# Optimization experiments

Hardware: AMD Instinct MI355X
Metric: run time of the kernel (lower is better)

Reference implementation:

```python
import jax, jax.numpy as jnp
import numpy as np

H, DK = 8, 32
D_MODEL = H * DK  # 256
Q_DIM = K_DIM = V_DIM = 256
B, T, S = 4, 4, 1024
NEG = -1e10


def setup_inputs() -> dict:
    rng = jax.random.key(0)
    ks = jax.random.split(rng, 12)
    w = lambda k, shp: (jax.random.normal(k, shp, jnp.float32) * 0.02)
    return {
        "query": jax.random.normal(ks[0], (B, T, S, Q_DIM), jnp.float32),
        "key": jax.random.normal(ks[1], (B, T, S, K_DIM), jnp.float32),
        "value": jax.random.normal(ks[2], (B, T, S, V_DIM), jnp.float32),
        "mask": jax.random.randint(ks[3], (B, T), 1, S + 1),  # valid lengths in [1, S]
        "Wq": w(ks[4], (D_MODEL, Q_DIM)), "bq": jnp.zeros((D_MODEL,), jnp.float32),
        "Wk": w(ks[5], (D_MODEL, K_DIM)), "bk": jnp.zeros((D_MODEL,), jnp.float32),
        "Wv": w(ks[6], (D_MODEL, V_DIM)), "bv": jnp.zeros((D_MODEL,), jnp.float32),
        "Wo": w(ks[7], (Q_DIM, D_MODEL)), "bo": jnp.zeros((Q_DIM,), jnp.float32),
    }


def reference(query, key, value, mask, Wq, bq, Wk, bk, Wv, bv, Wo, bo):
    b, t, s, _ = query.shape
    # projections -> [B,T,h,S,d_k]
    def proj(x, W, bias):
        y = jnp.einsum('btsf,df->btsd', x, W) + bias
        return y.reshape(b, t, s, H, DK).transpose(0, 1, 3, 2, 4)
    q = proj(query, Wq, bq)
    k = proj(key, Wk, bk)
    v = proj(value, Wv, bv)
    # scores [B,T,h,S,S]
    scores = jnp.einsum('bthqd,bthkd->bthqk', q, k) / jnp.sqrt(jnp.float32(DK))
    # vectorized length mask: positions < len on both axes (replaces torch python loop)
    valid = jnp.arange(s)[None, None, :] < mask[:, :, None]        # [B,T,S]
    m = valid[:, :, None, :, None] & valid[:, :, None, None, :]    # [B,T,1,S,S]
    scores = jnp.where(m, scores, NEG)
    p = jax.nn.softmax(scores, axis=-1)
    x = jnp.einsum('bthqk,bthkd->bthqd', p, v)                     # [B,T,h,S,d_k]
    x = x.transpose(0, 1, 3, 2, 4).reshape(b, t, s, H * DK)
    return jnp.einsum('btsd,qd->btsq', x, Wo) + bo
```

## Files before the change

### kernel.cpp

```cpp
#include <hip/hip_runtime.h>

#define EXPC 0.25505654442163f

typedef __attribute__((ext_vector_type(8))) short bfrag;
typedef __attribute__((ext_vector_type(4))) float ffrag;
typedef __attribute__((ext_vector_type(8))) unsigned int u8v;
typedef __attribute__((ext_vector_type(4))) unsigned int u4v;
typedef __attribute__((ext_vector_type(2))) unsigned int u2v;

__device__ __forceinline__ short f2bf(float x) {
  union { float f; unsigned u; } v; v.f = x;
  return (short)((v.u + 0x8000u) >> 16);
}

__device__ __forceinline__ unsigned int packbf(float a, float b) {
  return __builtin_amdgcn_perm(__float_as_uint(b) + 0x8000u,
                               __float_as_uint(a) + 0x8000u, 0x07060302u);
}

__device__ __forceinline__ bfrag cvtp(u8v x) {
  u4v r;
#pragma unroll
  for (int i = 0; i < 4; ++i)
    r[i] = __builtin_amdgcn_perm(x[2 * i + 1] + 0x8000u, x[2 * i] + 0x8000u, 0x07060302u);
  union { u4v u; bfrag b; } c; c.u = r; return c.b;
}
__device__ __forceinline__ bfrag cvt8(const float* __restrict__ p) {
  return cvtp(*(const u8v*)p);
}

__global__ __launch_bounds__(256, 4) void proj_kv(
    const float* __restrict__ kin, const float* __restrict__ Wk,
    const float* __restrict__ bk, const float* __restrict__ vin,
    const float* __restrict__ Wv, const float* __restrict__ bv,
    short* __restrict__ ko, short* __restrict__ vt) {
  const int t = threadIdx.x;
  const int lane = t & 63, wid = t >> 6;
  const int lrow = lane & 15, lq = lane >> 4;
  __shared__ __align__(16) char lds[18432];
  const int row4 = t >> 2, c4 = (t & 3) * 8;

  const bool isK = blockIdx.x < 512;
  if (isK) {
    const int bx = blockIdx.x >> 1, d0 = (blockIdx.x & 1) * 128;
    const int m0 = bx * 64;
    short* Ab = (short*)lds;
    short* Bb = (short*)(lds + 5120);
    short* tile = (short*)lds;
    ffrag acc[4][2] = {};
    u8v pa, pb0, pb1;
    pa  = *(const u8v*)(kin + (size_t)(m0 + row4) * 256 + c4);
    pb0 = *(const u8v*)(Wk + (size_t)(d0 + row4) * 256 + c4);
    pb1 = *(const u8v*)(Wk + (size_t)(d0 + 64 + row4) * 256 + c4);
    *(bfrag*)(Ab + row4 * 40 + c4) = cvtp(pa);
    *(bfrag*)(Bb + row4 * 40 + c4) = cvtp(pb0);
    *(bfrag*)(Bb + (64 + row4) * 40 + c4) = cvtp(pb1);
#pragma unroll 1
    for (int s = 0; s < 8; ++s) {
      __syncthreads();
      if (s < 7) {
        const int k1 = (s + 1) * 32;
        pa  = *(const u8v*)(kin + (size_t)(m0 + row4) * 256 + k1 + c4);
        pb0 = *(const u8v*)(Wk + (size_t)(d0 + row4) * 256 + k1 + c4);
        pb1 = *(const u8v*)(Wk + (size_t)(d0 + 64 + row4) * 256 + k1 + c4);
      }
      bfrag a[4], b[2];
#pragma unroll
      for (int i = 0; i < 4; ++i)
        a[i] = *(const bfrag*)(Ab + (i * 16 + lrow) * 40 + lq * 8);
#pragma unroll
      for (int j = 0; j < 2; ++j)
        b[j] = *(const bfrag*)(Bb + (wid * 32 + j * 16 + lrow) * 40 + lq * 8);
#pragma unroll
      for (int i = 0; i < 4; ++i)
#pragma unroll
        for (int j = 0; j < 2; ++j)
          acc[i][j] = __builtin_amdgcn_mfma_f32_16x16x32_bf16(a[i], b[j], acc[i][j], 0, 0, 0);
      __syncthreads();
      if (s < 7) {
        *(bfrag*)(Ab + row4 * 40 + c4) = cvtp(pa);
        *(bfrag*)(Bb + row4 * 40 + c4) = cvtp(pb0);
        *(bfrag*)(Bb + (64 + row4) * 40 + c4) = cvtp(pb1);
      }
    }
    __syncthreads();
#pragma unroll
    for (int j = 0; j < 2; ++j) {
      int dl = wid * 32 + j * 16 + lrow;
      float bs = bk[d0 + dl];
#pragma unroll
      for (int i = 0; i < 4; ++i)
#pragma unroll
        for (int r = 0; r < 4; ++r)
          tile[(i * 16 + lq * 4 + r) * 136 + dl] = f2bf(acc[i][j][r] + bs);
    }
    __syncthreads();
#pragma unroll
    for (int p = 0; p < 4; ++p) {
      int id2 = p * 256 + t;
      int row = id2 >> 4, c = id2 & 15;
      bfrag v = *(const bfrag*)(tile + row * 136 + c * 8);
      *(bfrag*)(ko + (size_t)(m0 + row) * 256 + d0 + c * 8) = v;
    }
  } else {
    const int t2 = blockIdx.x - 512;
    const int bx = t2 >> 1, d0 = (t2 & 1) * 128;
    const int n0 = bx * 64;
    short* Aw = (short*)lds;
    short* Bv = (short*)(lds + 10240);
    short* tile = (short*)lds;
    ffrag acc[2][4] = {};
    u8v pv, pw0, pw1;
    pw0 = *(const u8v*)(Wv + (size_t)(d0 + row4) * 256 + c4);
    pw1 = *(const u8v*)(Wv + (size_t)(d0 + 64 + row4) * 256 + c4);
    pv  = *(const u8v*)(vin + (size_t)(n0 + row4) * 256 + c4);
    *(bfrag*)(Aw + row4 * 40 + c4) = cvtp(pw0);
    *(bfrag*)(Aw + (64 + row4) * 40 + c4) = cvtp(pw1);
    *(bfrag*)(Bv + row4 * 40 + c4) = cvtp(pv);
#pragma unroll 1
    for (int s = 0; s < 8; ++s) {
      __syncthreads();
      if (s < 7) {
        const int k1 = (s + 1) * 32;
        pw0 = *(const u8v*)(Wv + (size_t)(d0 + row4) * 256 + k1 + c4);
        pw1 = *(const u8v*)(Wv + (size_t)(d0 + 64 + row4) * 256 + k1 + c4);
        pv  = *(const u8v*)(vin + (size_t)(n0 + row4) * 256 + k1 + c4);
      }
      bfrag a[2], b[4];
#pragma unroll
      for (int i = 0; i < 2; ++i)
        a[i] = *(const bfrag*)(Aw + (wid * 32 + i * 16 + lrow) * 40 + lq * 8);
#pragma unroll
      for (int j = 0; j < 4; ++j)
        b[j] = *(const bfrag*)(Bv + (j * 16 + lrow) * 40 + lq * 8);
#pragma unroll
      for (int i = 0; i < 2; ++i)
#pragma unroll
        for (int j = 0; j < 4; ++j)
          acc[i][j] = __builtin_amdgcn_mfma_f32_16x16x32_bf16(a[i], b[j], acc[i][j], 0, 0, 0);
      __syncthreads();
      if (s < 7) {
        *(bfrag*)(Aw + row4 * 40 + c4) = cvtp(pw0);
        *(bfrag*)(Aw + (64 + row4) * 40 + c4) = cvtp(pw1);
        *(bfrag*)(Bv + row4 * 40 + c4) = cvtp(pv);
      }
    }
    __syncthreads();
#pragma unroll
    for (int i = 0; i < 2; ++i)
#pragma unroll
      for (int r = 0; r < 4; ++r) {
        int dl = wid * 32 + i * 16 + lq * 4 + r;
        float bs = bv[d0 + dl];
#pragma unroll
        for (int j = 0; j < 4; ++j)
          tile[dl * 72 + j * 16 + lrow] = f2bf(acc[i][j][r] + bs);
      }
    __syncthreads();
    const int bt = n0 >> 10, sl0 = n0 & 1023;
#pragma unroll
    for (int p = 0; p < 4; ++p) {
      int id2 = p * 256 + t;
      int dl = id2 >> 3, c = id2 & 7;
      bfrag v = *(const bfrag*)(tile + dl * 72 + c * 8);
      *(bfrag*)(vt + (size_t)bt * 262144 + (size_t)(d0 + dl) * 1024 + sl0 + c * 8) = v;
    }
  }
}

__global__ __launch_bounds__(512, 4) void attn_fused(
    const float* __restrict__ query, const float* __restrict__ Wq,
    const float* __restrict__ bq, const float* __restrict__ Wo,
    const float* __restrict__ bo, const short* __restrict__ K,
    const short* __restrict__ Vt, const int* __restrict__ mask,
    float* __restrict__ out) {
  const int lane = threadIdx.x & 63, wid = threadIdx.x >> 6;
  const int lrow = lane & 15, lq = lane >> 4;
  const int id = blockIdx.x;
  const int bt = (id + (id >> 8)) & 15;
  const int q0 = (id >> 4) * 32;
  const int L = mask[bt];
  const int h = wid;

  __shared__ __align__(16) short qx[32 * 264];
  __shared__ __align__(16) unsigned int ptbuf[8][16 * 36];
  unsigned int* ptg = &ptbuf[wid][0];

  {
    const int n0 = h * 32;
    const float* X = query + ((size_t)bt * 1024 + q0) * 256;
    ffrag acc[2][2] = {};
    u8v xa[2], wb[2], xa_n[2], wb_n[2];
#pragma unroll
    for (int i = 0; i < 2; ++i)
      xa[i] = *(const u8v*)(X + (size_t)(i * 16 + lrow) * 256 + lq * 8);
#pragma unroll
    for (int j = 0; j < 2; ++j)
      wb[j] = *(const u8v*)(Wq + (size_t)(n0 + j * 16 + lrow) * 256 + lq * 8);
#pragma unroll 1
    for (int tt = 0; tt < 8; ++tt) {
      if (tt < 7) {
        const int kk = (tt + 1) * 32;
#pragma unroll
        for (int i = 0; i < 2; ++i)
          xa_n[i] = *(const u8v*)(X + (size_t)(i * 16 + lrow) * 256 + kk + lq * 8);
#pragma unroll
        for (int j = 0; j < 2; ++j)
          wb_n[j] = *(const u8v*)(Wq + (size_t)(n0 + j * 16 + lrow) * 256 + kk + lq * 8);
      }
      bfrag a[2], b[2];
#pragma unroll
      for (int i = 0; i < 2; ++i) a[i] = cvtp(xa[i]);
#pragma unroll
      for (int j = 0; j < 2; ++j) b[j] = cvtp(wb[j]);
#pragma unroll
      for (int i = 0; i < 2; ++i)
#pragma unroll
        for (int j = 0; j < 2; ++j)
          acc[i][j] = __builtin_amdgcn_mfma_f32_16x16x32_bf16(a[i], b[j], acc[i][j], 0, 0, 0);
#pragma unroll
      for (int i = 0; i < 2; ++i) xa[i] = xa_n[i];
#pragma unroll
      for (int j = 0; j < 2; ++j) wb[j] = wb_n[j];
    }
#pragma unroll
    for (int j = 0; j < 2; ++j) {
      int d = n0 + j * 16 + lrow;
      float bs = bq[d];
#pragma unroll
      for (int i = 0; i < 2; ++i)
#pragma unroll
        for (int r = 0; r < 4; ++r)
          qx[(i * 16 + lq * 4 + r) * 264 + d] = f2bf((acc[i][j][r] + bs) * EXPC);
    }
  }

  const short* Kb = K + (size_t)bt * 262144;
  const short* Vb = Vt + ((size_t)bt * 8 + h) * 32768;
  bfrag qf[2];
#pragma unroll
  for (int g = 0; g < 2; ++g)
    qf[g] = *(const bfrag*)(qx + (g * 16 + lrow) * 264 + h * 32 + lq * 8);

  const int nvalid = min(max(L - q0, 0), 32);
  const int nchunk = (nvalid > 0) ? ((L + 63) >> 6) : 0;

  float l_loc[2] = {0.f, 0.f};
  ffrag o[2][2] = {};

  bfrag kf[4], kf_n[4];
  if (nchunk > 0) {
#pragma unroll
    for (int f = 0; f < 4; ++f)
      kf[f] = *(const bfrag*)(Kb + (size_t)(f * 16 + lrow) * 256 + h * 32 + lq * 8);
  }

#pragma unroll 1
  for (int c = 0; c < nchunk; ++c) {
    const int kc = c * 64;
    const ffrag zf = {0.f, 0.f, 0.f, 0.f};
    if (c + 1 < nchunk) {
#pragma unroll
      for (int f = 0; f < 4; ++f)
        kf_n[f] = *(const bfrag*)(Kb + (size_t)(kc + 64 + f * 16 + lrow) * 256 + h * 32 + lq * 8);
    }
    bfrag av[2][2];
#pragma unroll
    for (int dj = 0; dj < 2; ++dj)
#pragma unroll
      for (int b = 0; b < 2; ++b)
        av[dj][b] = *(const bfrag*)(Vb + (size_t)(dj * 16 + lrow) * 1024 + kc + b * 32 + lq * 8);

    ffrag st[2][4];
#pragma unroll
    for (int g = 0; g < 2; ++g)
#pragma unroll
      for (int f = 0; f < 4; ++f)
        st[g][f] = __builtin_amdgcn_mfma_f32_16x16x32_bf16(kf[f], qf[g], zf, 0, 0, 0);

    const bool fullc = (kc + 64 <= L);
#pragma unroll
    for (int g = 0; g < 2; ++g) {
      float p[4][4];
      if (fullc) {
#pragma unroll
        for (int f = 0; f < 4; ++f)
#pragma unroll
          for (int r = 0; r < 4; ++r) {
            p[f][r] = __builtin_amdgcn_exp2f(st[g][f][r]);
            l_loc[g] += p[f][r];
          }
      } else {
#pragma unroll
        for (int f = 0; f < 4; ++f)
#pragma unroll
          for (int r = 0; r < 4; ++r) {
            int kr = kc + f * 16 + lq * 4 + r;
            float pv = (kr < L) ? __builtin_amdgcn_exp2f(st[g][f][r]) : 0.f;
            p[f][r] = pv;
            l_loc[g] += pv;
          }
      }
#pragma unroll
      for (int f = 0; f < 4; ++f) {
        u2v w;
        w[0] = packbf(p[f][0], p[f][1]);
        w[1] = packbf(p[f][2], p[f][3]);
        *(u2v*)(ptg + lrow * 36 + 8 * f + 2 * lq) = w;
      }
#pragma unroll
      for (int b = 0; b < 2; ++b) {
        u4v pv = *(const u4v*)(ptg + lrow * 36 + 16 * b + 4 * lq);
        union { u4v u; bfrag bf; } pt; pt.u = pv;
#pragma unroll
        for (int dj = 0; dj < 2; ++dj)
          o[g][dj] = __builtin_amdgcn_mfma_f32_16x16x32_bf16(av[dj][b], pt.bf, o[g][dj], 0, 0, 0);
      }
    }
#pragma unroll
    for (int f = 0; f < 4; ++f) kf[f] = kf_n[f];
  }

  float l_i[2];
#pragma unroll
  for (int g = 0; g < 2; ++g) {
    float rs = l_loc[g];
    rs += __shfl_xor(rs, 16);
    rs += __shfl_xor(rs, 32);
    l_i[g] = rs;
  }

  if (nvalid < 32) {
#pragma unroll
    for (int g = 0; g < 2; ++g) {
      bool inv = (g * 16 + lrow) >= nvalid;
      if (inv) {
        l_i[g] = 1024.f;
#pragma unroll
        for (int dj = 0; dj < 2; ++dj)
#pragma unroll
          for (int r = 0; r < 4; ++r) o[g][dj][r] = 0.f;
      }
    }
    bfrag ind[2];
#pragma unroll
    for (int g = 0; g < 2; ++g) {
      short iv = ((g * 16 + lrow) >= nvalid) ? (short)0x3F80 : (short)0;
#pragma unroll
      for (int j = 0; j < 8; ++j) ind[g][j] = iv;
    }
    const bool g0 = (nvalid < 16);
#pragma unroll 2
    for (int kc = 0; kc < 1024; kc += 64) {
#pragma unroll
      for (int dj = 0; dj < 2; ++dj)
#pragma unroll
        for (int b = 0; b < 2; ++b) {
          bfrag av = *(const bfrag*)(Vb + (size_t)(dj * 16 + lrow) * 1024 + kc + b * 32 + lq * 8);
          if (g0)
            o[0][dj] = __builtin_amdgcn_mfma_f32_16x16x32_bf16(av, ind[0], o[0][dj], 0, 0, 0);
          o[1][dj] = __builtin_amdgcn_mfma_f32_16x16x32_bf16(av, ind[1], o[1][dj], 0, 0, 0);
        }
    }
  }

#pragma unroll
  for (int g = 0; g < 2; ++g) {
    float rcp = 1.0f / l_i[g];
#pragma unroll
    for (int dj = 0; dj < 2; ++dj) {
      u2v w;
      w[0] = packbf(o[g][dj][0] * rcp, o[g][dj][1] * rcp);
      w[1] = packbf(o[g][dj][2] * rcp, o[g][dj][3] * rcp);
      short* dst = qx + (g * 16 + lrow) * 264 + h * 32 + dj * 16 + lq * 4;
      *(u2v*)dst = w;
    }
  }
  __syncthreads();

  {
    const int n0 = h * 32;
    ffrag acc[2][2] = {};
    u8v wb[2], wb_n[2];
#pragma unroll
    for (int j = 0; j < 2; ++j)
      wb[j] = *(const u8v*)(Wo + (size_t)(n0 + j * 16 + lrow) * 256 + lq * 8);
#pragma unroll 1
    for (int tt = 0; tt < 8; ++tt) {
      const int k0 = tt * 32;
      if (tt < 7) {
#pragma unroll
        for (int j = 0; j < 2; ++j)
          wb_n[j] = *(const u8v*)(Wo + (size_t)(n0 + j * 16 + lrow) * 256 + k0 + 32 + lq * 8);
      }
      bfrag a[2], b[2];
#pragma unroll
      for (int i = 0; i < 2; ++i)
        a[i] = *(const bfrag*)(qx + (i * 16 + lrow) * 264 + k0 + lq * 8);
#pragma unroll
      for (int j = 0; j < 2; ++j) b[j] = cvtp(wb[j]);
#pragma unroll
      for (int i = 0; i < 2; ++i)
#pragma unroll
        for (int j = 0; j < 2; ++j)
          acc[i][j] = __builtin_amdgcn_mfma_f32_16x16x32_bf16(a[i], b[j], acc[i][j], 0, 0, 0);
#pragma unroll
      for (int j = 0; j < 2; ++j) wb[j] = wb_n[j];
    }
#pragma unroll
    for (int j = 0; j < 2; ++j) {
      int d = n0 + j * 16 + lrow;
      float bs = bo[d];
#pragma unroll
      for (int i = 0; i < 2; ++i)
#pragma unroll
        for (int r = 0; r < 4; ++r)
          out[((size_t)bt * 1024 + q0 + i * 16 + lq * 4 + r) * 256 + d] = acc[i][j][r] + bs;
    }
  }
}

extern "C" void kernel_launch(void* const* d_in, const int* in_sizes, int n_in,
                              void* d_out, int out_size, void* d_ws, size_t ws_size,
                              hipStream_t stream) {
  const float* query = (const float*)d_in[0];
  const float* key   = (const float*)d_in[1];
  const float* value = (const float*)d_in[2];
  const int*   mask  = (const int*)d_in[3];
  const float* Wq = (const float*)d_in[4];
  const float* bq = (const float*)d_in[5];
  const float* Wk = (const float*)d_in[6];
  const float* bk = (const float*)d_in[7];
  const float* Wv = (const float*)d_in[8];
  const float* bv = (const float*)d_in[9];
  const float* Wo = (const float*)d_in[10];
  const float* bo = (const float*)d_in[11];
  float* out = (float*)d_out;

  short* k_ws  = (short*)d_ws;
  short* vt_ws = k_ws + 4194304;

  proj_kv<<<dim3(1024), 256, 0, stream>>>(key, Wk, bk, value, Wv, bv, k_ws, vt_ws);
  attn_fused<<<dim3(512), 512, 0, stream>>>(query, Wq, bq, Wo, bo,
                                            k_ws, vt_ws, mask, out);
}
```

Baseline: 218.1 us.

## Skip fully-masked query tiles and broadcast the constant masked-row output from the last tile

Query tiles that lie entirely beyond the valid length now return early instead of running the Q projection, attention loop and output projection. Their output rows all equal the same value (the mean of V over all keys, projected through Wo plus bias). The last tile of each batch computes that value once and writes it to every masked row. This removes redundant work for masked rows, but it makes the last tile's block do a long serial store loop, which could become a tail. It also relies on all masked rows having identical output.

```diff
diff --git a/kernel.cpp b/kernel.cpp
--- a/kernel.cpp
+++ b/kernel.cpp
@@ -178,159 +178,167 @@
   const int lrow = lane & 15, lq = lane >> 4;
   const int id = blockIdx.x;
   const int bt = (id + (id >> 8)) & 15;
-  const int q0 = (id >> 4) * 32;
+  const int qt = id >> 4;
+  const int q0 = qt * 32;
   const int L = mask[bt];
   const int h = wid;
+  const bool isLast = (qt == 31);
+  const int nvalid = min(max(L - q0, 0), 32);
+
+  if (nvalid <= 0 && !isLast) return;
+  const bool colsumOnly = isLast && (nvalid <= 0);
 
   __shared__ __align__(16) short qx[32 * 264];
   __shared__ __align__(16) unsigned int ptbuf[8][16 * 36];
   unsigned int* ptg = &ptbuf[wid][0];
-
-  {
-    const int n0 = h * 32;
-    const float* X = query + ((size_t)bt * 1024 + q0) * 256;
-    ffrag acc[2][2] = {};
-    u8v xa[2], wb[2], xa_n[2], wb_n[2];
-#pragma unroll
-    for (int i = 0; i < 2; ++i)
-      xa[i] = *(const u8v*)(X + (size_t)(i * 16 + lrow) * 256 + lq * 8);
-#pragma unroll
-    for (int j = 0; j < 2; ++j)
-      wb[j] = *(const u8v*)(Wq + (size_t)(n0 + j * 16 + lrow) * 256 + lq * 8);
-#pragma unroll 1
-    for (int tt = 0; tt < 8; ++tt) {
-      if (tt < 7) {
-        const int kk = (tt + 1) * 32;
+  float* vbuf = (float*)&ptbuf[0][0];
+
+  const short* Vb = Vt + ((size_t)bt * 8 + h) * 32768;
+  float l_i[2];
+  ffrag o[2][2] = {};
+
+  if (!colsumOnly) {
+    {
+      const int n0 = h * 32;
+      const float* X = query + ((size_t)bt * 1024 + q0) * 256;
+      ffrag acc[2][2] = {};
+      u8v xa[2], wb[2], xa_n[2], wb_n[2];
+#pragma unroll
+      for (int i = 0; i < 2; ++i)
+        xa[i] = *(const u8v*)(X + (size_t)(i * 16 + lrow) * 256 + lq * 8);
+#pragma unroll
+      for (int j = 0; j < 2; ++j)
+        wb[j] = *(const u8v*)(Wq + (size_t)(n0 + j * 16 + lrow) * 256 + lq * 8);
+#pragma unroll 1
+      for (int tt = 0; tt < 8; ++tt) {
+        if (tt < 7) {
+          const int kk = (tt + 1) * 32;
+#pragma unroll
+          for (int i = 0; i < 2; ++i)
+            xa_n[i] = *(const u8v*)(X + (size_t)(i * 16 + lrow) * 256 + kk + lq * 8);
+#pragma unroll
+          for (int j = 0; j < 2; ++j)
+            wb_n[j] = *(const u8v*)(Wq + (size_t)(n0 + j * 16 + lrow) * 256 + kk + lq * 8);
+        }
+        bfrag a[2], b[2];
+#pragma unroll
+        for (int i = 0; i < 2; ++i) a[i] = cvtp(xa[i]);
+#pragma unroll
+        for (int j = 0; j < 2; ++j) b[j] = cvtp(wb[j]);
 #pragma unroll
         for (int i = 0; i < 2; ++i)
-          xa_n[i] = *(const u8v*)(X + (size_t)(i * 16 + lrow) * 256 + kk + lq * 8);
-#pragma unroll
-        for (int j = 0; j < 2; ++j)
-          wb_n[j] = *(const u8v*)(Wq + (size_t)(n0 + j * 16 + lrow) * 256 + kk + lq * 8);
-      }
-      bfrag a[2], b[2];
-#pragma unroll
-      for (int i = 0; i < 2; ++i) a[i] = cvtp(xa[i]);
-#pragma unroll
-      for (int j = 0; j < 2; ++j) b[j] = cvtp(wb[j]);
-#pragma unroll
-      for (int i = 0; i < 2; ++i)
-#pragma unroll
-        for (int j = 0; j < 2; ++j)
-          acc[i][j] = __builtin_amdgcn_mfma_f32_16x16x32_bf16(a[i], b[j], acc[i][j], 0, 0, 0);
-#pragma unroll
-      for (int i = 0; i < 2; ++i) xa[i] = xa_n[i];
-#pragma unroll
-      for (int j = 0; j < 2; ++j) wb[j] = wb_n[j];
-    }
-#pragma unroll
-    for (int j = 0; j < 2; ++j) {
-      int d = n0 + j * 16 + lrow;
-      float bs = bq[d];
-#pragma unroll
-      for (int i = 0; i < 2; ++i)
-#pragma unroll
-        for (int r = 0; r < 4; ++r)
-          qx[(i * 16 + lq * 4 + r) * 264 + d] = f2bf((acc[i][j][r] + bs) * EXPC);
-    }
-  }
-
-  const short* Kb = K + (size_t)bt * 262144;
-  const short* Vb = Vt + ((size_t)bt * 8 + h) * 32768;
-  bfrag qf[2];
-#pragma unroll
-  for (int g = 0; g < 2; ++g)
-    qf[g] = *(const bfrag*)(qx + (g * 16 + lrow) * 264 + h * 32 + lq * 8);
-
-  const int nvalid = min(max(L - q0, 0), 32);
-  const int nchunk = (nvalid > 0) ? ((L + 63) >> 6) : 0;
-
-  float l_loc[2] = {0.f, 0.f};
-  ffrag o[2][2] = {};
-
-  bfrag kf[4], kf_n[4];
-  if (nchunk > 0) {
+#pragma unroll
+          for (int j = 0; j < 2; ++j)
+            acc[i][j] = __builtin_amdgcn_mfma_f32_16x16x32_bf16(a[i], b[j], acc[i][j], 0, 0, 0);
+#pragma unroll
+        for (int i = 0; i < 2; ++i) xa[i] = xa_n[i];
+#pragma unroll
+        for (int j = 0; j < 2; ++j) wb[j] = wb_n[j];
+      }
+#pragma unroll
+      for (int j = 0; j < 2; ++j) {
+        int d = n0 + j * 16 + lrow;
+        float bs = bq[d];
+#pragma unroll
+        for (int i = 0; i < 2; ++i)
+#pragma unroll
+          for (int r = 0; r < 4; ++r)
+            qx[(i * 16 + lq * 4 + r) * 264 + d] = f2bf((acc[i][j][r] + bs) * EXPC);
+      }
+    }
+
+    const short* Kb = K + (size_t)bt * 262144;
+    bfrag qf[2];
+#pragma unroll
+    for (int g = 0; g < 2; ++g)
+      qf[g] = *(const bfrag*)(qx + (g * 16 + lrow) * 264 + h * 32 + lq * 8);
+
+    const int nchunk = (L + 63) >> 6;
+    float l_loc[2] = {0.f, 0.f};
+    bfrag kf[4], kf_n[4];
 #pragma unroll
     for (int f = 0; f < 4; ++f)
       kf[f] = *(const bfrag*)(Kb + (size_t)(f * 16 + lrow) * 256 + h * 32 + lq * 8);
+
+#pragma unroll 1
+    for (int c = 0; c < nchunk; ++c) {
+      const int kc = c * 64;
+      const ffrag zf = {0.f, 0.f, 0.f, 0.f};
+      if (c + 1 < nchunk) {
+#pragma unroll
+        for (int f = 0; f < 4; ++f)
+          kf_n[f] = *(const bfrag*)(Kb + (size_t)(kc + 64 + f * 16 + lrow) * 256 + h * 32 + lq * 8);
+      }
+      bfrag av[2][2];
+#pragma unroll
+      for (int dj = 0; dj < 2; ++dj)
+#pragma unroll
+        for (int b = 0; b < 2; ++b)
+          av[dj][b] = *(const bfrag*)(Vb + (size_t)(dj * 16 + lrow) * 1024 + kc + b * 32 + lq * 8);
+
+      ffrag st[2][4];
+#pragma unroll
+      for (int g = 0; g < 2; ++g)
+#pragma unroll
+        for (int f = 0; f < 4; ++f)
+          st[g][f] = __builtin_amdgcn_mfma_f32_16x16x32_bf16(kf[f], qf[g], zf, 0, 0, 0);
+
+      const bool fullc = (kc + 64 <= L);
+#pragma unroll
+      for (int g = 0; g < 2; ++g) {
+        float p[4][4];
+        if (fullc) {
+#pragma unroll
+          for (int f = 0; f < 4; ++f)
+#pragma unroll
+            for (int r = 0; r < 4; ++r) {
+              p[f][r] = __builtin_amdgcn_exp2f(st[g][f][r]);
+              l_loc[g] += p[f][r];
+            }
+        } else {
+#pragma unroll
+          for (int f = 0; f < 4; ++f)
+#pragma unroll
+            for (int r = 0; r < 4; ++r) {
+              int kr = kc + f * 16 + lq * 4 + r;
+              float pv = (kr < L) ? __builtin_amdgcn_exp2f(st[g][f][r]) : 0.f;
+              p[f][r] = pv;
+              l_loc[g] += pv;
+            }
+        }
+#pragma unroll
+        for (int f = 0; f < 4; ++f) {
+          u2v w;
+          w[0] = packbf(p[f][0], p[f][1]);
+          w[1] = packbf(p[f][2], p[f][3]);
+          *(u2v*)(ptg + lrow * 36 + 8 * f + 2 * lq) = w;
+        }
+#pragma unroll
+        for (int b = 0; b < 2; ++b) {
+          u4v pv = *(const u4v*)(ptg + lrow * 36 + 16 * b + 4 * lq);
+          union { u4v u; bfrag bf; } pt; pt.u = pv;
+#pragma unroll
+          for (int dj = 0; dj < 2; ++dj)
+            o[g][dj] = __builtin_amdgcn_mfma_f32_16x16x32_bf16(av[dj][b], pt.bf, o[g][dj], 0, 0, 0);
+        }
+      }
+#pragma unroll
+      for (int f = 0; f < 4; ++f) kf[f] = kf_n[f];
+    }
+
+#pragma unroll
+    for (int g = 0; g < 2; ++g) {
+      float rs = l_loc[g];
+      rs += __shfl_xor(rs, 16);
+      rs += __shfl_xor(rs, 32);
+      l_i[g] = rs;
+    }
+  } else {
+#pragma unroll
+    for (int g = 0; g < 2; ++g) l_i[g] = 1024.f;
   }
 
-#pragma unroll 1
-  for (int c = 0; c < nchunk; ++c) {
-    const int kc = c * 64;
-    const ffrag zf = {0.f, 0.f, 0.f, 0.f};
-    if (c + 1 < nchunk) {
-#pragma unroll
-      for (int f = 0; f < 4; ++f)
-        kf_n[f] = *(const bfrag*)(Kb + (size_t)(kc + 64 + f * 16 + lrow) * 256 + h * 32 + lq * 8);
-    }
-    bfrag av[2][2];
-#pragma unroll
-    for (int dj = 0; dj < 2; ++dj)
-#pragma unroll
-      for (int b = 0; b < 2; ++b)
-        av[dj][b] = *(const bfrag*)(Vb + (size_t)(dj * 16 + lrow) * 1024 + kc + b * 32 + lq * 8);
-
-    ffrag st[2][4];
-#pragma unroll
-    for (int g = 0; g < 2; ++g)
-#pragma unroll
-      for (int f = 0; f < 4; ++f)
-        st[g][f] = __builtin_amdgcn_mfma_f32_16x16x32_bf16(kf[f], qf[g], zf, 0, 0, 0);
-
-    const bool fullc = (kc + 64 <= L);
-#pragma unroll
-    for (int g = 0; g < 2; ++g) {
-      float p[4][4];
-      if (fullc) {
-#pragma unroll
-        for (int f = 0; f < 4; ++f)
-#pragma unroll
-          for (int r = 0; r < 4; ++r) {
-            p[f][r] = __builtin_amdgcn_exp2f(st[g][f][r]);
-            l_loc[g] += p[f][r];
-          }
-      } else {
-#pragma unroll
-        for (int f = 0; f < 4; ++f)
-#pragma unroll
-          for (int r = 0; r < 4; ++r) {
-            int kr = kc + f * 16 + lq * 4 + r;
-            float pv = (kr < L) ? __builtin_amdgcn_exp2f(st[g][f][r]) : 0.f;
-            p[f][r] = pv;
-            l_loc[g] += pv;
-          }
-      }
-#pragma unroll
-      for (int f = 0; f < 4; ++f) {
-        u2v w;
-        w[0] = packbf(p[f][0], p[f][1]);
-        w[1] = packbf(p[f][2], p[f][3]);
-        *(u2v*)(ptg + lrow * 36 + 8 * f + 2 * lq) = w;
-      }
-#pragma unroll
-      for (int b = 0; b < 2; ++b) {
-        u4v pv = *(const u4v*)(ptg + lrow * 36 + 16 * b + 4 * lq);
-        union { u4v u; bfrag bf; } pt; pt.u = pv;
-#pragma unroll
-        for (int dj = 0; dj < 2; ++dj)
-          o[g][dj] = __builtin_amdgcn_mfma_f32_16x16x32_bf16(av[dj][b], pt.bf, o[g][dj], 0, 0, 0);
-      }
-    }
-#pragma unroll
-    for (int f = 0; f < 4; ++f) kf[f] = kf_n[f];
-  }
-
-  float l_i[2];
-#pragma unroll
-  for (int g = 0; g < 2; ++g) {
-    float rs = l_loc[g];
-    rs += __shfl_xor(rs, 16);
-    rs += __shfl_xor(rs, 32);
-    l_i[g] = rs;
-  }
-
-  if (nvalid < 32) {
+  if (isLast && nvalid < 32) {
 #pragma unroll
     for (int g = 0; g < 2; ++g) {
       bool inv = (g * 16 + lrow) >= nvalid;
@@ -407,15 +415,36 @@
 #pragma unroll
       for (int j = 0; j < 2; ++j) wb[j] = wb_n[j];
     }
-#pragma unroll
-    for (int j = 0; j < 2; ++j) {
-      int d = n0 + j * 16 + lrow;
-      float bs = bo[d];
-#pragma unroll
-      for (int i = 0; i < 2; ++i)
-#pragma unroll
-        for (int r = 0; r < 4; ++r)
-          out[((size_t)bt * 1024 + q0 + i * 16 + lq * 4 + r) * 256 + d] = acc[i][j][r] + bs;
+
+    if (!colsumOnly) {
+#pragma unroll
+      for (int j = 0; j < 2; ++j) {
+        int d = n0 + j * 16 + lrow;
+        float bs = bo[d];
+#pragma unroll
+        for (int i = 0; i < 2; ++i)
+#pragma unroll
+          for (int r = 0; r < 4; ++r) {
+            int qr = q0 + i * 16 + lq * 4 + r;
+            if (qr < L || isLast)
+              out[((size_t)bt * 1024 + qr) * 256 + d] = acc[i][j][r] + bs;
+          }
+      }
+    } else {
+      if (lq == 0) {
+#pragma unroll
+        for (int j = 0; j < 2; ++j) {
+          int d = n0 + j * 16 + lrow;
+          vbuf[d] = acc[0][j][0] + bo[d];
+        }
+      }
+      __syncthreads();
+      const int d = threadIdx.x & 255;
+      const float vv = vbuf[d];
+      float* ob = out + (size_t)bt * 1024 * 256 + d;
+#pragma unroll 1
+      for (int row = L + (threadIdx.x >> 8); row < 1024; row += 2)
+        ob[(size_t)row * 256] = vv;
     }
   }
 }
```

Result: faster. 204.3 us (-6.3%).
